# Kernel tuning notes

Measured on AMD Instinct MI355X. Metric: run time of the kernel, lower is better.

## Reference

```python
import jax, jax.numpy as jnp
import numpy as np

EMBED_DIM = 512
N_HEADS = 8
HEAD_DIM = EMBED_DIM // N_HEADS
MAX_H = 64
MAX_W = 48
B, H, W = 2, 64, 48


def setup_inputs() -> dict:
    key = jax.random.key(0)
    k1, k2, k3, k4, k5 = jax.random.split(key, 5)
    x = jax.random.normal(k1, (B, H, W, EMBED_DIM), dtype=jnp.float32)
    # Linear weights stored as [in, out] (torch stores [out, in]; math is x @ W_in_out)
    w_qkv = jax.random.normal(k2, (EMBED_DIM, 3 * EMBED_DIM), dtype=jnp.float32) * (EMBED_DIM ** -0.5)
    w_out = jax.random.normal(k3, (EMBED_DIM, EMBED_DIM), dtype=jnp.float32) * (EMBED_DIM ** -0.5)
    rel_row_tab = jax.random.normal(k4, (2 * MAX_H - 1, N_HEADS), dtype=jnp.float32) * 0.02
    rel_col_tab = jax.random.normal(k5, (2 * MAX_W - 1, N_HEADS), dtype=jnp.float32) * 0.02
    return {"x": x, "w_qkv": w_qkv, "w_out": w_out,
            "rel_row_tab": rel_row_tab, "rel_col_tab": rel_col_tab}


def _rel_bias(rel_row_tab, rel_col_tab, height, width):
    # 2D relative position bias: [n_heads, S, S]
    row_idx = jnp.repeat(jnp.arange(height), width)          # [S]
    col_idx = jnp.tile(jnp.arange(width), height)            # [S]
    rel_row = jnp.clip(row_idx[:, None] - row_idx[None, :] + MAX_H - 1, 0, 2 * MAX_H - 2)
    rel_col = jnp.clip(col_idx[:, None] - col_idx[None, :] + MAX_W - 1, 0, 2 * MAX_W - 2)
    bias = rel_row_tab[rel_row] + rel_col_tab[rel_col]       # [S, S, n_heads]
    return jnp.transpose(bias, (2, 0, 1))                    # [n_heads, S, S]


def reference(x, w_qkv, w_out, rel_row_tab, rel_col_tab):
    b, h, w, d = x.shape
    s = h * w
    x_flat = x.reshape(b, s, d)
    qkv = x_flat @ w_qkv                                     # [b, s, 3d]
    qkv = qkv.reshape(b, s, 3, N_HEADS, HEAD_DIM)
    qkv = jnp.transpose(qkv, (2, 0, 3, 1, 4))                # [3, b, nh, s, hd]
    q, k, v = qkv[0], qkv[1], qkv[2]
    scale = HEAD_DIM ** -0.5
    attn = jnp.einsum('bhqd,bhkd->bhqk', q, k) * scale       # [b, nh, s, s]
    attn = attn + _rel_bias(rel_row_tab, rel_col_tab, h, w)[None]
    attn = jax.nn.softmax(attn, axis=-1)
    out = jnp.einsum('bhqk,bhkd->bhqd', attn, v)             # [b, nh, s, hd]
    out = jnp.transpose(out, (0, 2, 1, 3)).reshape(b, s, d)
    out = out @ w_out
    return out.reshape(b, h, w, d)
```

## Files before the change

### kernel.cpp

```cpp
#include <hip/hip_runtime.h>
#include <hip/hip_bf16.h>

#define S_TOK 3072
#define NHEADS 8
#define KVT 12800

typedef __attribute__((ext_vector_type(8))) short short8;
typedef __attribute__((ext_vector_type(4))) float floatx4;
typedef __attribute__((ext_vector_type(4))) unsigned short ushortx4;

__device__ __forceinline__ unsigned short f2bf(float f) {
  union { float f; unsigned u; } v; v.f = f;
  unsigned r = v.u + 0x7fffu + ((v.u >> 16) & 1u);
  return (unsigned short)(r >> 16);
}
__device__ __forceinline__ float bf2f(unsigned short h) {
  union { unsigned u; float f; } v; v.u = (unsigned)h << 16;
  return v.f;
}
__device__ __forceinline__ unsigned pack2bf(float a, float b) {
  __hip_bfloat162 h = __float22bfloat162_rn(make_float2(a, b));
  union { __hip_bfloat162 h; unsigned u; } c; c.h = h;
  return c.u;
}
__device__ __forceinline__ void gload16(const void* g, void* l) {
  __builtin_amdgcn_global_load_lds(
      (const __attribute__((address_space(1))) unsigned int*)g,
      (__attribute__((address_space(3))) unsigned int*)l, 16, 0, 0);
}

__global__ __launch_bounds__(256) void ga_conv_all(
    const float* __restrict__ X, const float* __restrict__ Wq,
    const float* __restrict__ Wo, unsigned short* __restrict__ xh,
    unsigned short* __restrict__ xl, unsigned short* __restrict__ wqh,
    unsigned short* __restrict__ wql, unsigned short* __restrict__ woh,
    unsigned short* __restrict__ wol) {
  const int blk = blockIdx.x;
  const int t = threadIdx.x;
  if (blk < 1536) {
    const int c = blk * 256 + t;
    const int m = c >> 6;
    const int c8 = (c & 63) << 3;
    const float* src = X + (size_t)m * 512 + c8;
    float4 v0 = *(const float4*)src, v1 = *(const float4*)(src + 4);
    float vv[8] = {v0.x, v0.y, v0.z, v0.w, v1.x, v1.y, v1.z, v1.w};
    union { unsigned short s[8]; short8 v; } hh, ll;
#pragma unroll
    for (int e = 0; e < 8; ++e) {
      hh.s[e] = f2bf(vv[e]);
      ll.s[e] = f2bf(vv[e] - bf2f(hh.s[e]));
    }
    const size_t dst = (size_t)m * 512 + (c8 ^ ((m & 7) << 3));
    *(short8*)&xh[dst] = hh.v;
    *(short8*)&xl[dst] = ll.v;
    return;
  }
  const int wq = (blk < 1728);
  const int b2 = wq ? (blk - 1536) : (blk - 1728);
  const int N = wq ? 1536 : 512;
  const float* W = wq ? Wq : Wo;
  unsigned short* th = wq ? wqh : woh;
  unsigned short* tl = wq ? wql : wol;
  const int k0 = (b2 & 7) * 64, n0 = (b2 >> 3) * 64;
  __shared__ float Ts[64][65];
#pragma unroll
  for (int i = 0; i < 4; ++i) {
    const int r = (t >> 4) + i * 16, c4 = (t & 15) * 4;
    float4 v = *(const float4*)&W[(size_t)(k0 + r) * N + n0 + c4];
    Ts[r][c4] = v.x; Ts[r][c4 + 1] = v.y; Ts[r][c4 + 2] = v.z; Ts[r][c4 + 3] = v.w;
  }
  __syncthreads();
#pragma unroll
  for (int j = 0; j < 2; ++j) {
    const int chunk = t * 2 + j;
    const int nl = chunk >> 3, m8 = chunk & 7;
    const int n = n0 + nl;
    const int ks = (m8 * 8) ^ ((n & 7) << 3);
    union { unsigned short s[8]; short8 v; } hh, ll;
#pragma unroll
    for (int e = 0; e < 8; ++e) {
      float f = Ts[ks + e][nl];
      hh.s[e] = f2bf(f);
      ll.s[e] = f2bf(f - bf2f(hh.s[e]));
    }
    const size_t dst = (size_t)n * 512 + k0 + m8 * 8;
    *(short8*)&th[dst] = hh.v;
    *(short8*)&tl[dst] = ll.v;
  }
}

template <int BM, int BN>
__global__ __launch_bounds__(256, 2) void ga_mm3(
    const unsigned short* __restrict__ Ah, const unsigned short* __restrict__ Al,
    const unsigned short* __restrict__ Bh, const unsigned short* __restrict__ Bl,
    unsigned short* __restrict__ Qd, unsigned short* __restrict__ KV,
    unsigned short* __restrict__ Vd) {
  const int tid = threadIdx.x;
  const int w = tid >> 6, l = tid & 63;
  const int g = l >> 4, ln = l & 15;
  const int wm = w >> 1, wn = w & 1;
  const int m0 = blockIdx.x * BM;
  const int n0 = blockIdx.y * BN;
  constexpr int MI = BM / 32;
  constexpr int NI = BN / 32;
  __shared__ unsigned short Alds[2][BM * 64];
  __shared__ unsigned short Blds[2][BN * 64];
  floatx4 acc[MI][NI];
#pragma unroll
  for (int mi = 0; mi < MI; ++mi)
#pragma unroll
    for (int ni = 0; ni < NI; ++ni)
#pragma unroll
      for (int r = 0; r < 4; ++r) acc[mi][ni][r] = 0.f;

  for (int k0 = 0; k0 < 512; k0 += 64) {
    __syncthreads();
    {
      constexpr int PWA = (BM * 128) / 4096;
      constexpr int PWB = (BN * 128) / 4096;
      const char* ga_h = (const char*)(Ah + (size_t)m0 * 512 + k0);
      const char* ga_l = (const char*)(Al + (size_t)m0 * 512 + k0);
      const char* gb_h = (const char*)(Bh + (size_t)n0 * 512 + k0);
      const char* gb_l = (const char*)(Bl + (size_t)n0 * 512 + k0);
#pragma unroll
      for (int i = 0; i < PWA; ++i) {
        const int off = (w * PWA + i) * 1024;
        const int gb = ((off >> 7) + (l >> 3)) * 1024 + (l & 7) * 16;
        gload16(ga_h + gb, (char*)&Alds[0][0] + off);
        gload16(ga_l + gb, (char*)&Alds[1][0] + off);
      }
#pragma unroll
      for (int i = 0; i < PWB; ++i) {
        const int off = (w * PWB + i) * 1024;
        const int gb = ((off >> 7) + (l >> 3)) * 1024 + (l & 7) * 16;
        gload16(gb_h + gb, (char*)&Blds[0][0] + off);
        gload16(gb_l + gb, (char*)&Blds[1][0] + off);
      }
    }
    asm volatile("s_waitcnt vmcnt(0)" ::: "memory");
    __syncthreads();
#pragma unroll
    for (int kk = 0; kk < 64; kk += 32) {
      const int kbase = kk + g * 8;
      short8 ah[MI], al[MI], bh[NI], bl[NI];
#pragma unroll
      for (int mi = 0; mi < MI; ++mi) {
        const int row = wm * (BM / 2) + mi * 16 + ln;
        const int a = row * 64 + (kbase ^ ((row & 7) << 3));
        ah[mi] = *(const short8*)&Alds[0][a];
        al[mi] = *(const short8*)&Alds[1][a];
      }
#pragma unroll
      for (int ni = 0; ni < NI; ++ni) {
        const int row = wn * (BN / 2) + ni * 16 + ln;
        const int a = row * 64 + (kbase ^ ((row & 7) << 3));
        bh[ni] = *(const short8*)&Blds[0][a];
        bl[ni] = *(const short8*)&Blds[1][a];
      }
#pragma unroll
      for (int mi = 0; mi < MI; ++mi)
#pragma unroll
        for (int ni = 0; ni < NI; ++ni) {
          acc[mi][ni] = __builtin_amdgcn_mfma_f32_16x16x32_bf16(
              ah[mi], bh[ni], acc[mi][ni], 0, 0, 0);
          acc[mi][ni] = __builtin_amdgcn_mfma_f32_16x16x32_bf16(
              al[mi], bh[ni], acc[mi][ni], 0, 0, 0);
          acc[mi][ni] = __builtin_amdgcn_mfma_f32_16x16x32_bf16(
              ah[mi], bl[ni], acc[mi][ni], 0, 0, 0);
        }
    }
  }
  const int b = m0 / S_TOK;
  const int s_base = (m0 % S_TOK) + wm * (BM / 2);
#pragma unroll
  for (int ni = 0; ni < NI; ++ni) {
    const int ng = n0 + wn * (BN / 2) + ni * 16;
    const int which = ng >> 9;
    const int h = (ng >> 6) & 7;
    const int d = (ng & 63) + ln;
    const int bh = b * 8 + h;
    const float qs = (which == 0) ? 0.18033688f : 1.0f;
    if (which == 1) {
      unsigned short* kp = KV + (size_t)bh * 32 * KVT;
#pragma unroll
      for (int mi = 0; mi < MI; ++mi)
#pragma unroll
        for (int r = 0; r < 4; ++r) {
          const int s = s_base + mi * 16 + g * 4 + r;
          const int tile = s / 96;
          const int r96 = s - tile * 96;
          kp[tile * KVT + r96 * 64 + (d ^ ((s & 7) << 3))] =
              f2bf(acc[mi][ni][r]);
        }
    } else {
      unsigned short* hp =
          (which == 0 ? Qd : Vd) + (size_t)bh * S_TOK * 64;
#pragma unroll
      for (int mi = 0; mi < MI; ++mi)
#pragma unroll
        for (int r = 0; r < 4; ++r) {
          const int s = s_base + mi * 16 + g * 4 + r;
          hp[(size_t)s * 64 + d] = f2bf(acc[mi][ni][r] * qs);
        }
    }
  }
}

__global__ __launch_bounds__(256) void ga_vtrans(
    const unsigned short* __restrict__ V, unsigned short* __restrict__ KV) {
  const int t = threadIdx.x;
  const int tile = blockIdx.x;
  const int bh = blockIdx.y;
  __shared__ unsigned short Ts[96][72];
  const unsigned short* vp = V + ((size_t)bh * S_TOK + tile * 96) * 64;
#pragma unroll
  for (int it = 0; it < 3; ++it) {
    int c = it * 256 + t;
    int s = c >> 3, d8 = c & 7;
    short8 v = *(const short8*)&vp[(size_t)s * 64 + d8 * 8];
    *(short8*)&Ts[s][d8 * 8] = v;
  }
  __syncthreads();
  unsigned short* op = KV + ((size_t)bh * 32 + tile) * KVT + 6144;
#pragma unroll
  for (int it = 0; it < 4; ++it) {
    int c2 = it * 256 + t;
    if (c2 < 832) {
      const int d = c2 / 13;
      const int kc8 = (c2 - d * 13) * 8;
      short8 o;
      if (kc8 < 96) {
#pragma unroll
        for (int j = 0; j < 8; ++j) {
          const int p = kc8 + j;
          const int key =
              (p >> 5) * 32 + ((p >> 2) & 1) * 16 + ((p >> 3) & 3) * 4 + (p & 3);
          o[j] = (short)Ts[key][d];
        }
      } else {
#pragma unroll
        for (int j = 0; j < 8; ++j) o[j] = 0;
      }
      *(short8*)&op[d * 104 + kc8] = o;
    }
  }
}

__global__ __launch_bounds__(256) void ga_attn16(
    const unsigned short* __restrict__ Q, const unsigned short* __restrict__ KVg,
    const float* __restrict__ rowtab, const float* __restrict__ coltab,
    float* __restrict__ Opart, float* __restrict__ Lpart,
    int tiles_per_split) {
  const int tid = threadIdx.x;
  const int w = tid >> 6;
  const int l = tid & 63;
  const int g = l >> 4;
  const int ln = l & 15;
  const int bh = blockIdx.y;
  const int sp = blockIdx.z;
  const int h = bh & 7;
  const int q0 = blockIdx.x * 128 + w * 32;

  __shared__ float rtab[127];
  __shared__ float ctab[95];
  __shared__ unsigned short KVlds[2][KVT];
  for (int i = tid; i < 127; i += 256) rtab[i] = rowtab[i * 8 + h] * 1.44269504f;
  for (int i = tid; i < 95; i += 256) ctab[i] = coltab[i * 8 + h] * 1.44269504f;

  const unsigned short* Qp = Q + (size_t)bh * S_TOK * 64;
  const unsigned short* KVp = KVg + (size_t)bh * 32 * KVT;

  const int t0 = sp * tiles_per_split;
  const int tend = t0 + tiles_per_split;

  auto STAGE = [&](int b, int t) {
    const char* src = (const char*)(KVp + (size_t)t * KVT);
    char* dst = (char*)&KVlds[b][0];
#pragma unroll
    for (int i = 0; i < 6; ++i)
      gload16(src + i * 4096 + tid * 16, dst + i * 4096 + tid * 16);
    if (tid < 64) gload16(src + 24576 + tid * 16, dst + 24576 + tid * 16);
  };

  STAGE(0, t0);
  asm volatile("s_waitcnt vmcnt(0)" ::: "memory");
  __syncthreads();

  int qr[2], qc[2];
  short8 qf[2][2];
  float ctr[2][3][4];
#pragma unroll
  for (int u = 0; u < 2; ++u) {
    const int q = q0 + u * 16 + ln;
    qr[u] = q / 48;
    qc[u] = q - qr[u] * 48;
    qf[u][0] = *(const short8*)&Qp[(size_t)q * 64 + g * 8];
    qf[u][1] = *(const short8*)&Qp[(size_t)q * 64 + 32 + g * 8];
    const float* cb = &ctab[qc[u] - g * 4 + 47];
#pragma unroll
    for (int m = 0; m < 3; ++m)
#pragma unroll
      for (int r = 0; r < 4; ++r) ctr[u][m][r] = cb[-(16 * m + r)];
  }

  short8 ones;
  {
    union { unsigned short s[8]; short8 v; } on;
#pragma unroll
    for (int j = 0; j < 8; ++j) on.s[j] = 0x3F80;
    ones = on.v;
  }

  floatx4 o_acc[2][4];
  floatx4 o5[2];
#pragma unroll
  for (int u = 0; u < 2; ++u) {
#pragma unroll
    for (int r = 0; r < 4; ++r) o5[u][r] = 0.f;
#pragma unroll
    for (int dt = 0; dt < 4; ++dt)
#pragma unroll
      for (int r = 0; r < 4; ++r) o_acc[u][dt][r] = 0.f;
  }

  int cur = 0;
  for (int t = t0; t < tend; ++t) {
    if (t + 1 < tend) STAGE(cur ^ 1, t + 1);
    const unsigned short* kb = &KVlds[cur][0];
    const unsigned short* vb = &KVlds[cur][6144];
    float rt[2][2];
#pragma unroll
    for (int u = 0; u < 2; ++u) {
      rt[u][0] = rtab[qr[u] + 63 - 2 * t] - 12.0f;
      rt[u][1] = rtab[qr[u] + 62 - 2 * t] - 12.0f;
    }
    const int swz = (ln & 7) << 3;
#pragma unroll
    for (int kc32 = 0; kc32 < 3; ++kc32) {
      float e[2][2][4];
#pragma unroll
      for (int kh = 0; kh < 2; ++kh) {
        const int kt = kc32 * 2 + kh;
        const int rb = (kt * 16 + ln) * 64;
        short8 kf0 = *(const short8*)&kb[rb + ((g * 8) ^ swz)];
        short8 kf1 = *(const short8*)&kb[rb + ((32 + g * 8) ^ swz)];
        const int m = kt % 3, wrap = kt / 3;
#pragma unroll
        for (int u = 0; u < 2; ++u) {
          floatx4 s = {0.f, 0.f, 0.f, 0.f};
          s = __builtin_amdgcn_mfma_f32_16x16x32_bf16(kf0, qf[u][0], s, 0, 0, 0);
          s = __builtin_amdgcn_mfma_f32_16x16x32_bf16(kf1, qf[u][1], s, 0, 0, 0);
          const float rtw = rt[u][wrap];
#pragma unroll
          for (int r = 0; r < 4; ++r)
            e[u][kh][r] = __builtin_amdgcn_exp2f(s[r] + rtw + ctr[u][m][r]);
        }
      }
      short8 pf[2];
#pragma unroll
      for (int u = 0; u < 2; ++u) {
        union { unsigned uu[4]; short8 v; } pk;
        pk.uu[0] = pack2bf(e[u][0][0], e[u][0][1]);
        pk.uu[1] = pack2bf(e[u][0][2], e[u][0][3]);
        pk.uu[2] = pack2bf(e[u][1][0], e[u][1][1]);
        pk.uu[3] = pack2bf(e[u][1][2], e[u][1][3]);
        pf[u] = pk.v;
      }
#pragma unroll
      for (int dt = 0; dt < 4; ++dt) {
        const int vrow = dt * 16 + ln;
        short8 vf = *(const short8*)&vb[vrow * 104 + kc32 * 32 + g * 8];
        o_acc[0][dt] =
            __builtin_amdgcn_mfma_f32_16x16x32_bf16(pf[0], vf, o_acc[0][dt], 0, 0, 0);
        o_acc[1][dt] =
            __builtin_amdgcn_mfma_f32_16x16x32_bf16(pf[1], vf, o_acc[1][dt], 0, 0, 0);
      }
      o5[0] = __builtin_amdgcn_mfma_f32_16x16x32_bf16(pf[0], ones, o5[0], 0, 0, 0);
      o5[1] = __builtin_amdgcn_mfma_f32_16x16x32_bf16(pf[1], ones, o5[1], 0, 0, 0);
    }
    asm volatile("s_waitcnt vmcnt(0)" ::: "memory");
    __syncthreads();
    cur ^= 1;
  }
  const size_t rowbase = (size_t)(sp * 16 + bh) * S_TOK;
#pragma unroll
  for (int u = 0; u < 2; ++u) {
    if (ln == 0) {
#pragma unroll
      for (int r = 0; r < 4; ++r)
        Lpart[rowbase + q0 + u * 16 + g * 4 + r] = o5[u][r];
    }
#pragma unroll
    for (int dt = 0; dt < 4; ++dt)
#pragma unroll
      for (int r = 0; r < 4; ++r)
        Opart[(rowbase + q0 + u * 16 + g * 4 + r) * 64 + dt * 16 + ln] =
            o_acc[u][dt][r];
  }
}

template <int NS>
__global__ __launch_bounds__(256, 2) void ga_outmm(
    const float* __restrict__ Opart, const float* __restrict__ Lpart,
    const unsigned short* __restrict__ Bh_, float* __restrict__ Out) {
  const int tid = threadIdx.x;
  const int w = tid >> 6, l = tid & 63;
  const int g = l >> 4, ln = l & 15;
  const int wm = w >> 1, wn = w & 1;
  const int m0 = blockIdx.x * 64;
  const int n0 = blockIdx.y * 64;
  __shared__ unsigned short Alds[64 * 64];
  __shared__ unsigned short Blds[64 * 64];
  floatx4 acc[2][2];
#pragma unroll
  for (int mi = 0; mi < 2; ++mi)
#pragma unroll
    for (int ni = 0; ni < 2; ++ni)
#pragma unroll
      for (int r = 0; r < 4; ++r) acc[mi][ni][r] = 0.f;

  const int lm = tid >> 2, lk4 = tid & 3;
  const int m = m0 + lm;
  const int b = (m >= S_TOK) ? 1 : 0;
  const int q = m - b * S_TOK;

  for (int h = 0; h < 8; ++h) {
    __syncthreads();
    {
      const char* gb = (const char*)(Bh_ + (size_t)n0 * 512 + h * 64);
#pragma unroll
      for (int i = 0; i < 2; ++i) {
        const int off = (w * 2 + i) * 1024;
        const int gbo = ((off >> 7) + (l >> 3)) * 1024 + (l & 7) * 16;
        gload16(gb + gbo, (char*)Blds + off);
      }
    }
    {
      const int bh = b * 8 + h;
      float v[16];
      float ls = 0.f;
#pragma unroll
      for (int s = 0; s < NS; ++s) {
        const size_t row = (size_t)(s * 16 + bh) * S_TOK + q;
        ls += Lpart[row];
        const float* op = &Opart[row * 64 + lk4 * 16];
#pragma unroll
        for (int j = 0; j < 4; ++j) {
          float4 o = *(const float4*)(op + j * 4);
          if (s == 0) {
            v[j * 4] = o.x; v[j * 4 + 1] = o.y;
            v[j * 4 + 2] = o.z; v[j * 4 + 3] = o.w;
          } else {
            v[j * 4] += o.x; v[j * 4 + 1] += o.y;
            v[j * 4 + 2] += o.z; v[j * 4 + 3] += o.w;
          }
        }
      }
      const float inv = 1.0f / ls;
      unsigned pk[8];
#pragma unroll
      for (int j = 0; j < 8; ++j)
        pk[j] = pack2bf(v[2 * j] * inv, v[2 * j + 1] * inv);
      const int sw = (lm & 7) << 3;
      unsigned short* ab = &Alds[lm * 64];
#pragma unroll
      for (int j = 0; j < 4; ++j)
        *(uint2*)&ab[(lk4 * 16 + j * 4) ^ sw] = make_uint2(pk[2 * j], pk[2 * j + 1]);
    }
    asm volatile("s_waitcnt vmcnt(0)" ::: "memory");
    __syncthreads();
#pragma unroll
    for (int kk = 0; kk < 64; kk += 32) {
      const int kbase = kk + g * 8;
      short8 af[2], bf[2];
#pragma unroll
      for (int mi = 0; mi < 2; ++mi) {
        const int row = wm * 32 + mi * 16 + ln;
        af[mi] = *(const short8*)&Alds[row * 64 + (kbase ^ ((row & 7) << 3))];
      }
#pragma unroll
      for (int ni = 0; ni < 2; ++ni) {
        const int row = wn * 32 + ni * 16 + ln;
        bf[ni] = *(const short8*)&Blds[row * 64 + (kbase ^ ((row & 7) << 3))];
      }
#pragma unroll
      for (int mi = 0; mi < 2; ++mi)
#pragma unroll
        for (int ni = 0; ni < 2; ++ni)
          acc[mi][ni] = __builtin_amdgcn_mfma_f32_16x16x32_bf16(
              af[mi], bf[ni], acc[mi][ni], 0, 0, 0);
    }
  }
#pragma unroll
  for (int mi = 0; mi < 2; ++mi)
#pragma unroll
    for (int ni = 0; ni < 2; ++ni)
#pragma unroll
      for (int r = 0; r < 4; ++r)
        Out[(size_t)(m0 + wm * 32 + mi * 16 + g * 4 + r) * 512 + n0 +
            wn * 32 + ni * 16 + ln] = acc[mi][ni][r];
}

extern "C" void kernel_launch(void* const* d_in, const int* in_sizes, int n_in,
                              void* d_out, int out_size, void* d_ws,
                              size_t ws_size, hipStream_t stream) {
  const float* x = (const float*)d_in[0];
  const float* w_qkv = (const float*)d_in[1];
  const float* w_out = (const float*)d_in[2];
  const float* rrow = (const float*)d_in[3];
  const float* rcol = (const float*)d_in[4];
  float* out = (float*)d_out;

  unsigned short* ws16 = (unsigned short*)d_ws;
  unsigned short* xh = ws16;
  unsigned short* xl = xh + 3145728;
  unsigned short* wqh = xl + 3145728;
  unsigned short* wql = wqh + 786432;
  unsigned short* woh = wql + 786432;
  unsigned short* wol = woh + 262144;
  unsigned short* Qb = wol + 262144;
  unsigned short* Vb = Qb + 3145728;
  unsigned short* KV = Vb + 3145728;
  float* Opart = (float*)(KV + 6553600);
  const size_t base_bytes =
      ((size_t)3145728 * 4 + 786432 * 2 + 262144 * 2 + 6553600) * 2;
  const size_t per_split = (size_t)(3145728 + 49152) * 4;
  const int nsplit = (ws_size >= base_bytes + 2 * per_split) ? 2 : 1;
  float* Lpart = Opart + (size_t)nsplit * 3145728;

  ga_conv_all<<<1792, 256, 0, stream>>>(x, w_qkv, w_out, xh, xl, wqh, wql, woh,
                                        wol);
  ga_mm3<128, 128><<<dim3(48, 12), 256, 0, stream>>>(
      xh, xl, wqh, wql, Qb, KV, Vb);
  ga_vtrans<<<dim3(32, 16), 256, 0, stream>>>(Vb, KV);
  ga_attn16<<<dim3(24, 16, nsplit), 256, 0, stream>>>(
      Qb, KV, rrow, rcol, Opart, Lpart, 32 / nsplit);
  if (nsplit == 2)
    ga_outmm<2><<<dim3(96, 8), 256, 0, stream>>>(Opart, Lpart, woh, out);
  else
    ga_outmm<1><<<dim3(96, 8), 256, 0, stream>>>(Opart, Lpart, woh, out);
}
```

Before: 126.1 us.

## Prefetch next head's partials and double-buffer B tiles in out-projection

```diff
diff --git a/kernel.cpp b/kernel.cpp
--- a/kernel.cpp
+++ b/kernel.cpp
@@ -347,13 +347,14 @@
         const int m = kt % 3, wrap = kt / 3;
 #pragma unroll
         for (int u = 0; u < 2; ++u) {
-          floatx4 s = {0.f, 0.f, 0.f, 0.f};
+          floatx4 s;
+#pragma unroll
+          for (int r = 0; r < 4; ++r) s[r] = rt[u][wrap] + ctr[u][m][r];
           s = __builtin_amdgcn_mfma_f32_16x16x32_bf16(kf0, qf[u][0], s, 0, 0, 0);
           s = __builtin_amdgcn_mfma_f32_16x16x32_bf16(kf1, qf[u][1], s, 0, 0, 0);
-          const float rtw = rt[u][wrap];
 #pragma unroll
           for (int r = 0; r < 4; ++r)
-            e[u][kh][r] = __builtin_amdgcn_exp2f(s[r] + rtw + ctr[u][m][r]);
+            e[u][kh][r] = __builtin_amdgcn_exp2f(s[r]);
         }
       }
       short8 pf[2];
@@ -410,7 +411,7 @@
   const int m0 = blockIdx.x * 64;
   const int n0 = blockIdx.y * 64;
   __shared__ unsigned short Alds[64 * 64];
-  __shared__ unsigned short Blds[64 * 64];
+  __shared__ unsigned short Blds[2][64 * 64];
   floatx4 acc[2][2];
 #pragma unroll
   for (int mi = 0; mi < 2; ++mi)
@@ -424,51 +425,63 @@
   const int b = (m >= S_TOK) ? 1 : 0;
   const int q = m - b * S_TOK;
 
+  float v[16];
+  float ls;
+  auto ALOAD = [&](int h) {
+    const int bh = b * 8 + h;
+    ls = 0.f;
+#pragma unroll
+    for (int s = 0; s < NS; ++s) {
+      const size_t row = (size_t)(s * 16 + bh) * S_TOK + q;
+      ls += Lpart[row];
+      const float* op = &Opart[row * 64 + lk4 * 16];
+#pragma unroll
+      for (int j = 0; j < 4; ++j) {
+        float4 o = *(const float4*)(op + j * 4);
+        if (s == 0) {
+          v[j * 4] = o.x; v[j * 4 + 1] = o.y;
+          v[j * 4 + 2] = o.z; v[j * 4 + 3] = o.w;
+        } else {
+          v[j * 4] += o.x; v[j * 4 + 1] += o.y;
+          v[j * 4 + 2] += o.z; v[j * 4 + 3] += o.w;
+        }
+      }
+    }
+  };
+  auto BISSUE = [&](int h, int buf) {
+    const char* gb = (const char*)(Bh_ + (size_t)n0 * 512 + h * 64);
+#pragma unroll
+    for (int i = 0; i < 2; ++i) {
+      const int off = (w * 2 + i) * 1024;
+      const int gbo = ((off >> 7) + (l >> 3)) * 1024 + (l & 7) * 16;
+      gload16(gb + gbo, (char*)&Blds[buf][0] + off);
+    }
+  };
+  auto AWRITE = [&]() {
+    const float inv = 1.0f / ls;
+    unsigned pk[8];
+#pragma unroll
+    for (int j = 0; j < 8; ++j)
+      pk[j] = pack2bf(v[2 * j] * inv, v[2 * j + 1] * inv);
+    const int sw = (lm & 7) << 3;
+    unsigned short* ab = &Alds[lm * 64];
+#pragma unroll
+    for (int j = 0; j < 4; ++j)
+      *(uint2*)&ab[(lk4 * 16 + j * 4) ^ sw] = make_uint2(pk[2 * j], pk[2 * j + 1]);
+  };
+
+  ALOAD(0);
+  BISSUE(0, 0);
+  AWRITE();
+  asm volatile("s_waitcnt vmcnt(0)" ::: "memory");
+  __syncthreads();
+
+  int cur = 0;
   for (int h = 0; h < 8; ++h) {
-    __syncthreads();
-    {
-      const char* gb = (const char*)(Bh_ + (size_t)n0 * 512 + h * 64);
-#pragma unroll
-      for (int i = 0; i < 2; ++i) {
-        const int off = (w * 2 + i) * 1024;
-        const int gbo = ((off >> 7) + (l >> 3)) * 1024 + (l & 7) * 16;
-        gload16(gb + gbo, (char*)Blds + off);
-      }
-    }
-    {
-      const int bh = b * 8 + h;
-      float v[16];
-      float ls = 0.f;
-#pragma unroll
-      for (int s = 0; s < NS; ++s) {
-        const size_t row = (size_t)(s * 16 + bh) * S_TOK + q;
-        ls += Lpart[row];
-        const float* op = &Opart[row * 64 + lk4 * 16];
-#pragma unroll
-        for (int j = 0; j < 4; ++j) {
-          float4 o = *(const float4*)(op + j * 4);
-          if (s == 0) {
-            v[j * 4] = o.x; v[j * 4 + 1] = o.y;
-            v[j * 4 + 2] = o.z; v[j * 4 + 3] = o.w;
-          } else {
-            v[j * 4] += o.x; v[j * 4 + 1] += o.y;
-            v[j * 4 + 2] += o.z; v[j * 4 + 3] += o.w;
-          }
-        }
-      }
-      const float inv = 1.0f / ls;
-      unsigned pk[8];
-#pragma unroll
-      for (int j = 0; j < 8; ++j)
-        pk[j] = pack2bf(v[2 * j] * inv, v[2 * j + 1] * inv);
-      const int sw = (lm & 7) << 3;
-      unsigned short* ab = &Alds[lm * 64];
-#pragma unroll
-      for (int j = 0; j < 4; ++j)
-        *(uint2*)&ab[(lk4 * 16 + j * 4) ^ sw] = make_uint2(pk[2 * j], pk[2 * j + 1]);
-    }
-    asm volatile("s_waitcnt vmcnt(0)" ::: "memory");
-    __syncthreads();
+    if (h < 7) {
+      ALOAD(h + 1);
+      BISSUE(h + 1, cur ^ 1);
+    }
 #pragma unroll
     for (int kk = 0; kk < 64; kk += 32) {
       const int kbase = kk + g * 8;
@@ -481,7 +494,8 @@
 #pragma unroll
       for (int ni = 0; ni < 2; ++ni) {
         const int row = wn * 32 + ni * 16 + ln;
-        bf[ni] = *(const short8*)&Blds[row * 64 + (kbase ^ ((row & 7) << 3))];
+        bf[ni] =
+            *(const short8*)&Blds[cur][row * 64 + (kbase ^ ((row & 7) << 3))];
       }
 #pragma unroll
       for (int mi = 0; mi < 2; ++mi)
@@ -489,6 +503,12 @@
         for (int ni = 0; ni < 2; ++ni)
           acc[mi][ni] = __builtin_amdgcn_mfma_f32_16x16x32_bf16(
               af[mi], bf[ni], acc[mi][ni], 0, 0, 0);
+    }
+    if (h < 7) {
+      __syncthreads();
+      AWRITE();
+      __syncthreads();
+      cur ^= 1;
     }
   }
 #pragma unroll
```

Result: no change. 124.2 us (-1.5%).
